# Performance work log

Measured on AMD Instinct MI355X. Metric: run time of the kernel, lower is better.

## Reference

```python
import jax, jax.numpy as jnp
import numpy as np

P = 2; NH = 16; HS = 1024; NL = 12; NC = 1000
B, D, H, W = 32, 64, 32, 32
LFEAT = P * P * D  # 256 per-patch feature dim


def _sincos_1d(dim, pos):
    omega = np.arange(dim // 2, dtype=np.float64) / (dim / 2.0)
    omega = 1.0 / 10000 ** omega
    out = np.einsum('m,d->md', pos.reshape(-1), omega)
    return np.concatenate([np.sin(out), np.cos(out)], axis=1)


def _pos_embed(dim, grid_size):
    g = np.arange(grid_size, dtype=np.float32)
    grid = np.stack(np.meshgrid(g, g), axis=0).reshape(2, 1, grid_size, grid_size)
    emb = np.concatenate([_sincos_1d(dim // 2, grid[0]), _sincos_1d(dim // 2, grid[1])], axis=1)
    return jnp.asarray(emb, dtype=jnp.float32)


def setup_inputs() -> dict:
    key = jax.random.key(0)
    ks = iter(jax.random.split(key, 40))
    def w(shape, s=0.02):
        return jax.random.normal(next(ks), shape, jnp.float32) * s
    return {
        'x': jax.random.normal(next(ks), (B, D, H, W), jnp.float32),
        'y': jax.random.randint(next(ks), (B,), 0, NC),
        't': jax.random.randint(next(ks), (B,), 0, 1000),
        'proj_w': w((LFEAT, HS)), 'proj_b': jnp.zeros((HS,), jnp.float32),
        'pos_embed': _pos_embed(HS, H // P),
        'emb_table': w((NC + 1, HS)),
        'blk_mod_w': w((NL, HS, 6 * HS)), 'blk_mod_b': jnp.zeros((NL, 6 * HS), jnp.float32),
        'blk_wq': w((NL, HS, HS)), 'blk_bq': jnp.zeros((NL, HS), jnp.float32),
        'blk_wk': w((NL, HS, HS)), 'blk_bk': jnp.zeros((NL, HS), jnp.float32),
        'blk_wv': w((NL, HS, HS)), 'blk_bv': jnp.zeros((NL, HS), jnp.float32),
        'blk_wo': w((NL, HS, HS)), 'blk_bo': jnp.zeros((NL, HS), jnp.float32),
        'blk_fc1_w': w((NL, HS, 4 * HS)), 'blk_fc1_b': jnp.zeros((NL, 4 * HS), jnp.float32),
        'blk_fc2_w': w((NL, 4 * HS, HS)), 'blk_fc2_b': jnp.zeros((NL, HS), jnp.float32),
        'fin_mod_w': w((HS, 2 * HS)), 'fin_mod_b': jnp.zeros((2 * HS,), jnp.float32),
        'fin_out_w': w((HS, LFEAT)), 'fin_out_b': jnp.zeros((LFEAT,), jnp.float32),
    }


def _ln(z):
    mu = jnp.mean(z, -1, keepdims=True)
    var = jnp.mean((z - mu) ** 2, -1, keepdims=True)
    return (z - mu) * jax.lax.rsqrt(var + 1e-5)


def _forward(x, y, t, proj_w, proj_b, pos_embed, emb_table,
             blk_mod_w, blk_mod_b, blk_wq, blk_bq, blk_wk, blk_bk, blk_wv, blk_bv,
             blk_wo, blk_bo, blk_fc1_w, blk_fc1_b, blk_fc2_w, blk_fc2_b,
             fin_mod_w, fin_mod_b, fin_out_w, fin_out_b):
    Bc, Dc, Hc, Wc = x.shape
    Hp, Wp = Hc // P, Wc // P
    dh = HS // NH
    # patchify_flatten: (B, L, P*P*D)
    tok = x.reshape(Bc, Dc, Hp, P, Wp, P).transpose(0, 2, 4, 3, 5, 1).reshape(Bc, Hp * Wp, P * P * Dc)
    tok = tok @ proj_w + proj_b + pos_embed[None]
    # timestep_embedding: [cos, sin] order per source
    half = HS // 2
    freqs = jnp.exp(-jnp.log(jnp.float32(10000.0)) * jnp.arange(half, dtype=jnp.float32) / half)
    ang = t.astype(jnp.float32)[:, None] * freqs[None]
    c = jnp.concatenate([jnp.cos(ang), jnp.sin(ang)], axis=-1) + emb_table[y]
    c_act = jax.nn.silu(c)  # each block applies silu to c (c is not mutated across blocks)

    def block(xc, p):
        mw, mb, wq, bq, wk, bk, wv, bv, wo, bo, f1w, f1b, f2w, f2b = p
        mod = c_act @ mw + mb
        sh_a, sc_a, g_a, sh_m, sc_m, g_m = jnp.split(mod, 6, axis=1)
        hx = _ln(xc) * (1 + sc_a[:, None]) + sh_a[:, None]
        def heads(z, wz, bz):
            return (z @ wz + bz).reshape(Bc, -1, NH, dh).transpose(0, 2, 1, 3)
        q, k, v = heads(hx, wq, bq), heads(hx, wk, bk), heads(hx, wv, bv)
        logits = jnp.einsum('bhqd,bhkd->bhqk', q, k) / jnp.sqrt(jnp.float32(dh))
        # non-AR mask buffer is all zeros -> no-op
        attn = jax.nn.softmax(logits, axis=-1)
        o = jnp.einsum('bhqk,bhkd->bhqd', attn, v).transpose(0, 2, 1, 3).reshape(Bc, -1, HS)
        xc = xc + g_a[:, None] * (o @ wo + bo)
        hx = _ln(xc) * (1 + sc_m[:, None]) + sh_m[:, None]
        mlp = jax.nn.gelu(hx @ f1w + f1b, approximate=False) @ f2w + f2b
        return xc + g_m[:, None] * mlp, None

    tok, _ = jax.lax.scan(block, tok, (blk_mod_w, blk_mod_b, blk_wq, blk_bq, blk_wk, blk_bk,
                                       blk_wv, blk_bv, blk_wo, blk_bo,
                                       blk_fc1_w, blk_fc1_b, blk_fc2_w, blk_fc2_b))
    fmod = c_act @ fin_mod_w + fin_mod_b
    sh, sc = jnp.split(fmod, 2, axis=1)
    out = (_ln(tok) * (1 + sc[:, None]) + sh[:, None]) @ fin_out_w + fin_out_b
    # unpatchify -> (B, D, H, W)
    return out.reshape(Bc, Hp, Wp, P, P, Dc).transpose(0, 5, 1, 3, 2, 4).reshape(Bc, Dc, Hc, Wc)


def reference(x, y, t, proj_w, proj_b, pos_embed, emb_table,
              blk_mod_w, blk_mod_b, blk_wq, blk_bq, blk_wk, blk_bk, blk_wv, blk_bv,
              blk_wo, blk_bo, blk_fc1_w, blk_fc1_b, blk_fc2_w, blk_fc2_b,
              fin_mod_w, fin_mod_b, fin_out_w, fin_out_b):
    return _forward(x, y, t, proj_w, proj_b, pos_embed, emb_table,
                    blk_mod_w, blk_mod_b, blk_wq, blk_bq, blk_wk, blk_bk, blk_wv, blk_bv,
                    blk_wo, blk_bo, blk_fc1_w, blk_fc1_b, blk_fc2_w, blk_fc2_b,
                    fin_mod_w, fin_mod_b, fin_out_w, fin_out_b)
```

## Files before the change

kernel.cpp:

```cpp
#include <hip/hip_runtime.h>
#include <hip/hip_bf16.h>
#include <math.h>

typedef short s16x8 __attribute__((ext_vector_type(8)));
typedef float f32x4 __attribute__((ext_vector_type(4)));
typedef unsigned short u16;

__device__ __forceinline__ u16 f2b(float f) {
    unsigned u = __builtin_bit_cast(unsigned, f);
    u += 0x7fffu + ((u >> 16) & 1u);
    return (u16)(u >> 16);
}
__device__ __forceinline__ f32x4 mfma16(s16x8 a, s16x8 b, f32x4 c) {
    return __builtin_amdgcn_mfma_f32_16x16x32_bf16(a, b, c, 0, 0, 0);
}
__device__ __forceinline__ void gload16(const void* g, void* l) {
    __builtin_amdgcn_global_load_lds((const __attribute__((address_space(1))) unsigned*)g,
                                     (__attribute__((address_space(3))) unsigned*)l, 16, 0, 0);
}

__global__ __launch_bounds__(256) void patchify_kernel(const float* __restrict__ x, u16* __restrict__ out) {
    int idx = blockIdx.x * 256 + threadIdx.x;
    int row = idx >> 8, col = idx & 255;
    int b = row >> 8, ll = row & 255, hp = ll >> 4, wp = ll & 15;
    int pp = col >> 6, d = col & 63;
    out[idx] = f2b(x[(size_t)((b * 64 + d) * 32 + hp * 2 + (pp >> 1)) * 32 + wp * 2 + (pp & 1)]);
}

__global__ __launch_bounds__(256) void cact_kernel(const int* __restrict__ t, const int* __restrict__ y,
                                                   const float* __restrict__ emb, u16* __restrict__ cact) {
    int b = blockIdx.x, tid = threadIdx.x;
    float tv = (float)t[b];
    int yb = y[b];
#pragma unroll
    for (int j = 0; j < 4; ++j) {
        int c = tid * 4 + j;
        int f = (c < 512) ? c : c - 512;
        float freq = __expf(-9.210340371976184f * (float)f * (1.f / 512.f));
        float ang = tv * freq;
        float v = (c < 512) ? cosf(ang) : sinf(ang);
        v += emb[(size_t)yb * 1024 + c];
        v = v / (1.f + __expf(-v));
        cact[b * 1024 + c] = f2b(v);
    }
}

__global__ __launch_bounds__(256) void bcat_kernel(const float* __restrict__ bq, const float* __restrict__ bk,
                                                   const float* __restrict__ bv, float* __restrict__ out) {
    int lyr = blockIdx.x, j = blockIdx.y, tid = threadIdx.x;
    const float* src = (j == 0) ? bq : ((j == 1) ? bk : bv);
    float4 v = ((const float4*)(src + (size_t)lyr * 1024))[tid];
    ((float4*)(out + (size_t)lyr * 3072 + j * 1024))[tid] = v;
}

__device__ __forceinline__ void tpose_body(float (*tile)[65], const float* __restrict__ in,
                                           u16* __restrict__ out, int R, int C, int r0, int c0, int tid) {
    int rr = tid >> 4, cc = (tid & 15) * 4;
#pragma unroll
    for (int j = 0; j < 4; ++j) {
        float4 v = *(const float4*)&in[(size_t)(r0 + j * 16 + rr) * C + c0 + cc];
        tile[j * 16 + rr][cc]     = v.x;
        tile[j * 16 + rr][cc + 1] = v.y;
        tile[j * 16 + rr][cc + 2] = v.z;
        tile[j * 16 + rr][cc + 3] = v.w;
    }
    __syncthreads();
    int oc = tid >> 3, r8 = (tid & 7) * 8;
#pragma unroll
    for (int j = 0; j < 2; ++j) {
        int ocl = j * 32 + oc;
        s16x8 vv;
#pragma unroll
        for (int e = 0; e < 8; ++e) vv[e] = (short)f2b(tile[r8 + e][ocl]);
        *(s16x8*)&out[(size_t)(c0 + ocl) * R + r0 + r8] = vv;
    }
}

__global__ __launch_bounds__(256) void transpose_cvt64k(const float* __restrict__ in, u16* __restrict__ out,
                                                        int R, int C) {
    __shared__ float tile[64][65];
    tpose_body(tile, in, out, R, C, blockIdx.y * 64, blockIdx.x * 64, threadIdx.x);
}

__global__ __launch_bounds__(256) void transpose_layer(
    const float* __restrict__ mw, const float* __restrict__ wq, const float* __restrict__ wk,
    const float* __restrict__ wv, const float* __restrict__ wo, const float* __restrict__ f1,
    const float* __restrict__ f2,
    u16* __restrict__ modT, u16* __restrict__ qkvT, u16* __restrict__ woT,
    u16* __restrict__ f1T, u16* __restrict__ f2T) {
    __shared__ float tile[64][65];
    int bid = blockIdx.x, tid = threadIdx.x;
    const float* src; u16* dst; int R, C, tloc;
    if (bid < 1536)      { src = mw; dst = modT;               R = 1024; C = 6144; tloc = bid; }
    else if (bid < 1792) { src = wq; dst = qkvT;               R = 1024; C = 1024; tloc = bid - 1536; }
    else if (bid < 2048) { src = wk; dst = qkvT + 1024 * 1024; R = 1024; C = 1024; tloc = bid - 1792; }
    else if (bid < 2304) { src = wv; dst = qkvT + 2048 * 1024; R = 1024; C = 1024; tloc = bid - 2048; }
    else if (bid < 2560) { src = wo; dst = woT;                R = 1024; C = 1024; tloc = bid - 2304; }
    else if (bid < 3584) { src = f1; dst = f1T;                R = 1024; C = 4096; tloc = bid - 2560; }
    else                 { src = f2; dst = f2T;                R = 4096; C = 1024; tloc = bid - 3584; }
    int tx = C >> 6;
    int ty = tloc / tx, txi = tloc - ty * tx;
    tpose_body(tile, src, dst, R, C, ty * 64, txi * 64, tid);
}

__global__ __launch_bounds__(256) void ln_mod_kernel(const float* __restrict__ x, const float* __restrict__ modv,
                                                     int mod_ld, int sh_off, int sc_off, u16* __restrict__ out) {
    int row = blockIdx.x, tid = threadIdx.x, b = row >> 8;
    float4 xv = ((const float4*)(x + (size_t)row * 1024))[tid];
    float s = xv.x + xv.y + xv.z + xv.w;
    float s2 = xv.x * xv.x + xv.y * xv.y + xv.z * xv.z + xv.w * xv.w;
#pragma unroll
    for (int d = 1; d < 64; d <<= 1) { s += __shfl_xor(s, d); s2 += __shfl_xor(s2, d); }
    __shared__ float red[8];
    int w = tid >> 6;
    if ((tid & 63) == 0) { red[w] = s; red[4 + w] = s2; }
    __syncthreads();
    s = red[0] + red[1] + red[2] + red[3];
    s2 = red[4] + red[5] + red[6] + red[7];
    float mu = s * (1.f / 1024.f);
    float rs = rsqrtf(s2 * (1.f / 1024.f) - mu * mu + 1e-5f);
    const float* shp = modv + (size_t)b * mod_ld + sh_off;
    const float* scp = modv + (size_t)b * mod_ld + sc_off;
    float4 sh4 = ((const float4*)shp)[tid];
    float4 sc4 = ((const float4*)scp)[tid];
    u16 o0 = f2b((xv.x - mu) * rs * (1.f + sc4.x) + sh4.x);
    u16 o1 = f2b((xv.y - mu) * rs * (1.f + sc4.y) + sh4.y);
    u16 o2 = f2b((xv.z - mu) * rs * (1.f + sc4.z) + sh4.z);
    u16 o3 = f2b((xv.w - mu) * rs * (1.f + sc4.w) + sh4.w);
    unsigned long long pk = (unsigned long long)o0 | ((unsigned long long)o1 << 16) |
                            ((unsigned long long)o2 << 32) | ((unsigned long long)o3 << 48);
    *(unsigned long long*)&out[(size_t)row * 1024 + tid * 4] = pk;
}

template <int EPI>
__global__ __launch_bounds__(512, 1) void gemm8(
    const u16* __restrict__ A, int lda, const u16* __restrict__ Bt, int ldb,
    int M, int N, int K, const float* __restrict__ bias,
    float* __restrict__ outF, u16* __restrict__ outB, int ldc,
    const float* __restrict__ aux1, const float* __restrict__ aux2, int gateOff) {
    __shared__ u16 As[3][256 * 64];
    __shared__ u16 Bs[3][128 * 64];

    const int tid = threadIdx.x, w = tid >> 6, l = tid & 63;
    const int wm = w >> 1, wn = w & 1;

    const int nbn = N >> 7;
    const int nwg = gridDim.x;
    const int orig = blockIdx.x;
    const int cpx = nwg >> 3;
    const int wg = (orig & 7) * cpx + (orig >> 3);
    const int bm = wg / nbn, bn = wg - bm * nbn;
    const int row0 = bm << 8, col0 = bn << 7;

    const int NT = K >> 6;

    const int srow = tid >> 3, sslot = tid & 7;
    const int ksl = sslot ^ (((srow >> 2) & 1) << 1);
    const u16* gA = A + (size_t)(row0 + srow) * lda + ksl * 8;
    const u16* gB = Bt + (size_t)(col0 + srow) * ldb + ksl * 8;
    const int lOff = srow * 64 + sslot * 8;

    const int fr = l & 15, fg = l >> 4;
    const int arow = wm * 64 + fr;
    const int brow = wn * 64 + fr;

    f32x4 acc[4][4];
#pragma unroll
    for (int m = 0; m < 4; ++m)
#pragma unroll
        for (int n = 0; n < 4; ++n) acc[m][n] = (f32x4){0.f, 0.f, 0.f, 0.f};

    {
        u16* a0 = &As[0][lOff];
        u16* b0 = &Bs[0][lOff];
#pragma unroll
        for (int a = 0; a < 4; ++a) gload16(gA + (size_t)a * 64 * lda, a0 + a * 4096);
#pragma unroll
        for (int b = 0; b < 2; ++b) gload16(gB + (size_t)b * 64 * ldb, b0 + b * 4096);
        if (NT > 1) {
            u16* a1 = &As[1][lOff];
#pragma unroll
            for (int a = 0; a < 3; ++a) gload16(gA + (size_t)a * 64 * lda + 64, a1 + a * 4096);
        }
    }
    if (NT > 1) { asm volatile("s_waitcnt vmcnt(3)" ::: "memory"); }
    else        { asm volatile("s_waitcnt vmcnt(0)" ::: "memory"); }
    __builtin_amdgcn_s_barrier();
    __builtin_amdgcn_sched_barrier(0);

    int q = 0;
    for (int t = 0; t < NT; ++t) {
        const u16* ca = As[q];
        const u16* cb = Bs[q];
        const int q1 = (q == 2) ? 0 : q + 1;
        const int q2 = (q1 == 2) ? 0 : q1 + 1;

        s16x8 af[4][2], bf[4][2];
#pragma unroll
        for (int m = 0; m < 4; ++m) {
            int r = arow + m * 16;
            int psb = fg ^ (((r >> 2) & 1) << 1);
            af[m][0] = *(const s16x8*)(ca + r * 64 + psb * 8);
            af[m][1] = *(const s16x8*)(ca + r * 64 + psb * 8 + 32);
        }
#pragma unroll
        for (int n = 0; n < 2; ++n) {
            int r = brow + n * 16;
            int psb = fg ^ (((r >> 2) & 1) << 1);
            bf[n][0] = *(const s16x8*)(cb + r * 64 + psb * 8);
            bf[n][1] = *(const s16x8*)(cb + r * 64 + psb * 8 + 32);
        }
        if (t + 1 < NT) {
            gload16(gA + (size_t)(3 * 64) * lda + (size_t)(t + 1) * 64, &As[q1][lOff] + 3 * 4096);
            gload16(gB + (size_t)(t + 1) * 64, &Bs[q1][lOff]);
            gload16(gB + (size_t)(1 * 64) * ldb + (size_t)(t + 1) * 64, &Bs[q1][lOff] + 4096);
        }
        __builtin_amdgcn_s_barrier();
        __builtin_amdgcn_s_setprio(1);
#pragma unroll
        for (int m = 0; m < 4; ++m)
#pragma unroll
            for (int n = 0; n < 2; ++n) {
                acc[m][n] = mfma16(af[m][0], bf[n][0], acc[m][n]);
                acc[m][n] = mfma16(af[m][1], bf[n][1], acc[m][n]);
            }
        __builtin_amdgcn_s_setprio(0);
        __builtin_amdgcn_s_barrier();
#pragma unroll
        for (int n = 0; n < 2; ++n) {
            int r = brow + (n + 2) * 16;
            int psb = fg ^ (((r >> 2) & 1) << 1);
            bf[n + 2][0] = *(const s16x8*)(cb + r * 64 + psb * 8);
            bf[n + 2][1] = *(const s16x8*)(cb + r * 64 + psb * 8 + 32);
        }
        if (t + 2 < NT) {
#pragma unroll
            for (int a = 0; a < 3; ++a)
                gload16(gA + (size_t)a * 64 * lda + (size_t)(t + 2) * 64, &As[q2][lOff] + a * 4096);
        }
        __builtin_amdgcn_s_barrier();
        __builtin_amdgcn_s_setprio(1);
#pragma unroll
        for (int m = 0; m < 4; ++m)
#pragma unroll
            for (int n = 2; n < 4; ++n) {
                acc[m][n] = mfma16(af[m][0], bf[n][0], acc[m][n]);
                acc[m][n] = mfma16(af[m][1], bf[n][1], acc[m][n]);
            }
        __builtin_amdgcn_s_setprio(0);
        if (t < NT - 2)       { asm volatile("s_waitcnt vmcnt(3)" ::: "memory"); }
        else if (t == NT - 2) { asm volatile("s_waitcnt vmcnt(0)" ::: "memory"); }
        if (t < NT - 1) {
            __builtin_amdgcn_s_barrier();
            __builtin_amdgcn_sched_barrier(0);
        }
        q = q1;
    }

    const int erow = row0 + wm * 64 + fg * 4;
    const int ecol = col0 + wn * 64 + fr;
#pragma unroll
    for (int m = 0; m < 4; ++m) {
#pragma unroll
        for (int n = 0; n < 4; ++n) {
#pragma unroll
            for (int r = 0; r < 4; ++r) {
                int row = erow + m * 16 + r;
                int col = ecol + n * 16;
                float v = acc[m][n][r];
                if constexpr (EPI == 1) {
                    outB[(size_t)row * ldc + col] = f2b(v + bias[col]);
                } else if constexpr (EPI == 2) {
                    outF[(size_t)row * ldc + col] = v + bias[col] + aux1[(size_t)(row & 255) * 1024 + col];
                } else if constexpr (EPI == 3) {
                    outF[(size_t)row * ldc + col] =
                        aux1[(size_t)row * ldc + col] +
                        aux2[(size_t)(row >> 8) * 6144 + gateOff + col] * (v + bias[col]);
                } else {
                    float xg = v + bias[col];
                    outB[(size_t)row * ldc + col] = f2b(0.5f * xg * (1.f + erff(xg * 0.70710678118654752f)));
                }
            }
        }
    }
}

template <int EPI>
__global__ __launch_bounds__(256, 2) void gemm_k(
    const u16* __restrict__ A, int lda, const u16* __restrict__ Bt, int ldb,
    int M, int N, int K, const float* __restrict__ bias,
    float* outF, u16* __restrict__ outB, int ldc) {
    __shared__ u16 Asl[128 * 32];
    __shared__ u16 Bsl[128 * 32];
    const int tid = threadIdx.x, w = tid >> 6, l = tid & 63;
    const int row0 = blockIdx.y * 128, col0 = blockIdx.x * 128;
    const int wm = w >> 1, wn = w & 1;

    f32x4 acc[4][4];
#pragma unroll
    for (int m = 0; m < 4; ++m)
#pragma unroll
        for (int n = 0; n < 4; ++n) acc[m][n] = (f32x4){0.f, 0.f, 0.f, 0.f};

    const int rA0 = w * 16 + (l >> 2), rA1 = rA0 + 64;
    const int kc = (l & 3) * 8;
    int gr0 = row0 + rA0; if (gr0 > M - 1) gr0 = M - 1;
    int gr1 = row0 + rA1; if (gr1 > M - 1) gr1 = M - 1;
    const u16* a0 = A + (size_t)gr0 * lda + kc;
    const u16* a1 = A + (size_t)gr1 * lda + kc;
    const u16* b0 = Bt + (size_t)(col0 + rA0) * ldb + kc;
    const u16* b1 = Bt + (size_t)(col0 + rA1) * ldb + kc;
    u16* la0 = &Asl[rA0 * 32 + kc];
    u16* la1 = &Asl[rA1 * 32 + kc];
    u16* lb0 = &Bsl[rA0 * 32 + kc];
    u16* lb1 = &Bsl[rA1 * 32 + kc];

    for (int k0 = 0; k0 < K; k0 += 32) {
        __syncthreads();
        gload16(a0 + k0, la0);
        gload16(a1 + k0, la1);
        gload16(b0 + k0, lb0);
        gload16(b1 + k0, lb1);
        __syncthreads();
        s16x8 af[4], bfr[4];
#pragma unroll
        for (int m = 0; m < 4; ++m)
            af[m] = *(const s16x8*)&Asl[(wm * 64 + m * 16 + (l & 15)) * 32 + (l >> 4) * 8];
#pragma unroll
        for (int n = 0; n < 4; ++n)
            bfr[n] = *(const s16x8*)&Bsl[(wn * 64 + n * 16 + (l & 15)) * 32 + (l >> 4) * 8];
#pragma unroll
        for (int m = 0; m < 4; ++m)
#pragma unroll
            for (int n = 0; n < 4; ++n) acc[m][n] = mfma16(af[m], bfr[n], acc[m][n]);
    }

#pragma unroll
    for (int m = 0; m < 4; ++m) {
#pragma unroll
        for (int n = 0; n < 4; ++n) {
#pragma unroll
            for (int r = 0; r < 4; ++r) {
                int row = row0 + wm * 64 + m * 16 + (l >> 4) * 4 + r;
                if (row >= M) continue;
                int col = col0 + wn * 64 + n * 16 + (l & 15);
                float v = acc[m][n][r];
                if constexpr (EPI == 0) {
                    outF[(size_t)row * ldc + col] = v + bias[col];
                } else {
                    float xg = v + bias[col];
                    int bb = row >> 8, ll = row & 255, hp = ll >> 4, wp = ll & 15;
                    int pp = col >> 6, d = col & 63;
                    outF[(size_t)((bb * 64 + d) * 32 + hp * 2 + (pp >> 1)) * 32 + wp * 2 + (pp & 1)] = xg;
                }
            }
        }
    }
}

__global__ __launch_bounds__(256, 2) void attn_kernel(const u16* __restrict__ qkv, u16* __restrict__ obuf) {
    __shared__ u16 Qs[64 * 64];
    __shared__ u16 Ks[256 * 64];
    __shared__ u16 VTs[64 * 256];
    int qt = blockIdx.x, h = blockIdx.y, b = blockIdx.z;
    int tid = threadIdx.x, w = tid >> 6, l = tid & 63;
    size_t base = (size_t)b * 256 * 3072;

    {
        int r = tid >> 2;
#pragma unroll
        for (int j = 0; j < 2; ++j) {
            int sg = (tid & 3) + j * 4;
            *(s16x8*)&Qs[r * 64 + sg * 8] =
                *(const s16x8*)&qkv[base + (size_t)(qt * 64 + r) * 3072 + h * 64 + sg * 8];
        }
    }
#pragma unroll
    for (int j = 0; j < 8; ++j) {
        int i = tid + j * 256;
        int r = i >> 3, sg = i & 7;
        *(s16x8*)&Ks[r * 64 + sg * 8] =
            *(const s16x8*)&qkv[base + (size_t)r * 3072 + 1024 + h * 64 + sg * 8];
    }
#pragma unroll
    for (int j = 0; j < 8; ++j) {
        int i = tid + j * 256;
        int r = i >> 3, sg = i & 7;
        s16x8 v = *(const s16x8*)&qkv[base + (size_t)r * 3072 + 2048 + h * 64 + sg * 8];
#pragma unroll
        for (int e = 0; e < 8; ++e) VTs[(sg * 8 + e) * 256 + r] = ((const u16*)&v)[e];
    }
    __syncthreads();

    s16x8 aq0 = *(const s16x8*)&Qs[(w * 16 + (l & 15)) * 64 + (l >> 4) * 8];
    s16x8 aq1 = *(const s16x8*)&Qs[(w * 16 + (l & 15)) * 64 + 32 + (l >> 4) * 8];
    f32x4 sf[16];
#pragma unroll
    for (int cf = 0; cf < 16; ++cf) {
        f32x4 a = (f32x4){0.f, 0.f, 0.f, 0.f};
        s16x8 bk0 = *(const s16x8*)&Ks[(cf * 16 + (l & 15)) * 64 + (l >> 4) * 8];
        s16x8 bk1 = *(const s16x8*)&Ks[(cf * 16 + (l & 15)) * 64 + 32 + (l >> 4) * 8];
        a = mfma16(aq0, bk0, a);
        a = mfma16(aq1, bk1, a);
        sf[cf] = a * 0.125f;
    }
    __syncthreads();

#pragma unroll
    for (int r = 0; r < 4; ++r) {
        float m = -1e30f;
#pragma unroll
        for (int cf = 0; cf < 16; ++cf) m = fmaxf(m, sf[cf][r]);
#pragma unroll
        for (int d = 1; d < 16; d <<= 1) m = fmaxf(m, __shfl_xor(m, d));
        float sm = 0.f;
#pragma unroll
        for (int cf = 0; cf < 16; ++cf) { float e = __expf(sf[cf][r] - m); sf[cf][r] = e; sm += e; }
#pragma unroll
        for (int d = 1; d < 16; d <<= 1) sm += __shfl_xor(sm, d);
        float inv = 1.f / sm;
        int rl = w * 16 + (l >> 4) * 4 + r;
#pragma unroll
        for (int cf = 0; cf < 16; ++cf) Ks[rl * 256 + cf * 16 + (l & 15)] = f2b(sf[cf][r] * inv);
    }
    __syncthreads();

    f32x4 oacc[4];
#pragma unroll
    for (int cf = 0; cf < 4; ++cf) oacc[cf] = (f32x4){0.f, 0.f, 0.f, 0.f};
#pragma unroll
    for (int ks = 0; ks < 8; ++ks) {
        s16x8 ap = *(const s16x8*)&Ks[(w * 16 + (l & 15)) * 256 + ks * 32 + (l >> 4) * 8];
#pragma unroll
        for (int cf = 0; cf < 4; ++cf) {
            s16x8 bv = *(const s16x8*)&VTs[(cf * 16 + (l & 15)) * 256 + ks * 32 + (l >> 4) * 8];
            oacc[cf] = mfma16(ap, bv, oacc[cf]);
        }
    }
    size_t orow0 = (size_t)(b * 256 + qt * 64 + w * 16);
#pragma unroll
    for (int cf = 0; cf < 4; ++cf)
#pragma unroll
        for (int r = 0; r < 4; ++r) {
            int rr = (l >> 4) * 4 + r;
            obuf[(orow0 + rr) * 1024 + h * 64 + cf * 16 + (l & 15)] = f2b(oacc[cf][r]);
        }
}

extern "C" void kernel_launch(void* const* d_in, const int* in_sizes, int n_in,
                              void* d_out, int out_size, void* d_ws, size_t ws_size,
                              hipStream_t stream) {
    (void)in_sizes; (void)n_in; (void)out_size; (void)ws_size;
    const float* x         = (const float*)d_in[0];
    const int*   y         = (const int*)d_in[1];
    const int*   t         = (const int*)d_in[2];
    const float* proj_w    = (const float*)d_in[3];
    const float* proj_b    = (const float*)d_in[4];
    const float* pos_embed = (const float*)d_in[5];
    const float* emb_table = (const float*)d_in[6];
    const float* blk_mod_w = (const float*)d_in[7];
    const float* blk_mod_b = (const float*)d_in[8];
    const float* blk_wq    = (const float*)d_in[9];
    const float* blk_bq    = (const float*)d_in[10];
    const float* blk_wk    = (const float*)d_in[11];
    const float* blk_bk    = (const float*)d_in[12];
    const float* blk_wv    = (const float*)d_in[13];
    const float* blk_bv    = (const float*)d_in[14];
    const float* blk_wo    = (const float*)d_in[15];
    const float* blk_bo    = (const float*)d_in[16];
    const float* blk_f1w   = (const float*)d_in[17];
    const float* blk_f1b   = (const float*)d_in[18];
    const float* blk_f2w   = (const float*)d_in[19];
    const float* blk_f2b   = (const float*)d_in[20];
    const float* fin_mod_w = (const float*)d_in[21];
    const float* fin_mod_b = (const float*)d_in[22];
    const float* fin_out_w = (const float*)d_in[23];
    const float* fin_out_b = (const float*)d_in[24];
    float* out = (float*)d_out;

    char* ws = (char*)d_ws;
    size_t off = 0;
    auto alloc = [&](size_t bytes) -> char* {
        char* p = ws + off;
        off += (bytes + 255) & ~(size_t)255;
        return p;
    };
    float* xc    = (float*)alloc(8192ull * 1024 * 4);
    u16*   hx    = (u16*)alloc(8192ull * 1024 * 2);
    u16*   qkvb  = (u16*)alloc(8192ull * 3072 * 2);
    u16*   obufp = (u16*)alloc(8192ull * 1024 * 2);
    u16*   h1    = (u16*)alloc(8192ull * 4096 * 2);
    u16*   patchA= (u16*)alloc(8192ull * 256 * 2);
    u16*   cact  = (u16*)alloc(32ull * 1024 * 2);
    float* modb  = (float*)alloc(32ull * 6144 * 4);
    float* fmod  = (float*)alloc(32ull * 2048 * 4);
    float* bqkv  = (float*)alloc(12ull * 3072 * 4);
    u16*   projT = (u16*)alloc(1024ull * 256 * 2);
    u16*   fmT   = (u16*)alloc(2048ull * 1024 * 2);
    u16*   foT   = (u16*)alloc(256ull * 1024 * 2);
    u16*   modT  = (u16*)alloc(6144ull * 1024 * 2);
    u16*   qkvT  = (u16*)alloc(3072ull * 1024 * 2);
    u16*   woT   = (u16*)alloc(1024ull * 1024 * 2);
    u16*   f1T   = (u16*)alloc(4096ull * 1024 * 2);
    u16*   f2T   = (u16*)alloc(1024ull * 4096 * 2);

    patchify_kernel<<<8192, 256, 0, stream>>>(x, patchA);
    cact_kernel<<<32, 256, 0, stream>>>(t, y, emb_table, cact);
    bcat_kernel<<<dim3(12, 3), 256, 0, stream>>>(blk_bq, blk_bk, blk_bv, bqkv);
    transpose_cvt64k<<<dim3(16, 4), 256, 0, stream>>>(proj_w, projT, 256, 1024);
    transpose_cvt64k<<<dim3(32, 16), 256, 0, stream>>>(fin_mod_w, fmT, 1024, 2048);
    transpose_cvt64k<<<dim3(4, 16), 256, 0, stream>>>(fin_out_w, foT, 1024, 256);

    gemm8<2><<<256, 512, 0, stream>>>(patchA, 256, projT, 256, 8192, 1024, 256,
                                      proj_b, xc, nullptr, 1024, pos_embed, nullptr, 0);
    gemm_k<0><<<dim3(16, 1), 256, 0, stream>>>(cact, 1024, fmT, 1024, 32, 2048, 1024,
                                               fin_mod_b, fmod, nullptr, 2048);

    for (int i = 0; i < 12; ++i) {
        transpose_layer<<<4608, 256, 0, stream>>>(
            blk_mod_w + (size_t)i * 1024 * 6144,
            blk_wq + (size_t)i * 1024 * 1024, blk_wk + (size_t)i * 1024 * 1024,
            blk_wv + (size_t)i * 1024 * 1024, blk_wo + (size_t)i * 1024 * 1024,
            blk_f1w + (size_t)i * 1024 * 4096, blk_f2w + (size_t)i * 4096 * 1024,
            modT, qkvT, woT, f1T, f2T);

        gemm_k<0><<<dim3(48, 1), 256, 0, stream>>>(cact, 1024, modT, 1024, 32, 6144, 1024,
                                                   blk_mod_b + (size_t)i * 6144, modb, nullptr, 6144);
        ln_mod_kernel<<<8192, 256, 0, stream>>>(xc, modb, 6144, 0, 1024, hx);
        gemm8<1><<<768, 512, 0, stream>>>(hx, 1024, qkvT, 1024, 8192, 3072, 1024,
                                          bqkv + (size_t)i * 3072, nullptr, qkvb, 3072,
                                          nullptr, nullptr, 0);
        attn_kernel<<<dim3(4, 16, 32), 256, 0, stream>>>(qkvb, obufp);
        gemm8<3><<<256, 512, 0, stream>>>(obufp, 1024, woT, 1024, 8192, 1024, 1024,
                                          blk_bo + (size_t)i * 1024, xc, nullptr, 1024,
                                          xc, modb, 2048);
        ln_mod_kernel<<<8192, 256, 0, stream>>>(xc, modb, 6144, 3072, 4096, hx);
        gemm8<4><<<1024, 512, 0, stream>>>(hx, 1024, f1T, 1024, 8192, 4096, 1024,
                                           blk_f1b + (size_t)i * 4096, nullptr, h1, 4096,
                                           nullptr, nullptr, 0);
        gemm8<3><<<256, 512, 0, stream>>>(h1, 4096, f2T, 4096, 8192, 1024, 4096,
                                          blk_f2b + (size_t)i * 1024, xc, nullptr, 1024,
                                          xc, modb, 5120);
    }
    ln_mod_kernel<<<8192, 256, 0, stream>>>(xc, fmod, 2048, 0, 1024, hx);
    gemm_k<5><<<dim3(2, 64), 256, 0, stream>>>(hx, 1024, foT, 1024, 8192, 256, 1024,
                                               fin_out_b, out, nullptr, 256);
}
```

Measured before the change: 5.103 ms.

## Add 256x256 GEMM for QKV/FC1, fp32 mod GEMV, drop mod-weight transpose

Adds a gemm256 kernel with 256x256 tiles and K-step 32 for the QKV and FC1 projections, so each workgroup reuses more data per LDS load than the 256x128 gemm8. The adaLN modulation matmuls (M=32) move to a new fp32 mod32_kernel that reads the untransposed weights directly. This removes the per-layer transpose and bf16 conversion of the large 1024x6144 mod weight. gemm8's LDS swizzle changes to a full 8-slot XOR to cut bank conflicts. The fp32 GEMV is bandwidth bound and still reads the full fp32 weight; the larger tiles cut the number of workgroups.

```diff
diff --git a/kernel.cpp b/kernel.cpp
--- a/kernel.cpp
+++ b/kernel.cpp
@@ -28,7 +28,7 @@
 }
 
 __global__ __launch_bounds__(256) void cact_kernel(const int* __restrict__ t, const int* __restrict__ y,
-                                                   const float* __restrict__ emb, u16* __restrict__ cact) {
+                                                   const float* __restrict__ emb, float* __restrict__ cactF) {
     int b = blockIdx.x, tid = threadIdx.x;
     float tv = (float)t[b];
     int yb = y[b];
@@ -41,7 +41,7 @@
         float v = (c < 512) ? cosf(ang) : sinf(ang);
         v += emb[(size_t)yb * 1024 + c];
         v = v / (1.f + __expf(-v));
-        cact[b * 1024 + c] = f2b(v);
+        cactF[b * 1024 + c] = v;
     }
 }
 
@@ -53,6 +53,51 @@
     ((float4*)(out + (size_t)lyr * 3072 + j * 1024))[tid] = v;
 }
 
+__global__ __launch_bounds__(256) void mod32_kernel(const float* __restrict__ cactF, const float* __restrict__ W,
+                                                    const float* __restrict__ bias, float* __restrict__ out, int N) {
+    __shared__ float cs[32 * 256];
+    __shared__ float red[4 * 32 * 64];
+    int tid = threadIdx.x, lane = tid & 63, kg = tid >> 6;
+    int n = blockIdx.x * 64 + lane;
+    float acc[32];
+#pragma unroll
+    for (int r = 0; r < 32; ++r) acc[r] = 0.f;
+    for (int ch = 0; ch < 4; ++ch) {
+        __syncthreads();
+#pragma unroll
+        for (int j = 0; j < 8; ++j) {
+            int idx = tid * 4 + j * 1024;
+            float4 v = *(const float4*)&cactF[(size_t)(idx >> 8) * 1024 + ch * 256 + (idx & 255)];
+            *(float4*)&cs[idx] = v;
+        }
+        __syncthreads();
+        const float* Wp = W + (size_t)(ch * 256 + kg * 64) * N + n;
+        for (int kk = 0; kk < 64; kk += 4) {
+            float w0 = Wp[(size_t)(kk + 0) * N];
+            float w1 = Wp[(size_t)(kk + 1) * N];
+            float w2 = Wp[(size_t)(kk + 2) * N];
+            float w3 = Wp[(size_t)(kk + 3) * N];
+            int kb = kg * 64 + kk;
+#pragma unroll
+            for (int r = 0; r < 32; ++r) {
+                float4 cv = *(const float4*)&cs[r * 256 + kb];
+                acc[r] += cv.x * w0 + cv.y * w1 + cv.z * w2 + cv.w * w3;
+            }
+        }
+    }
+#pragma unroll
+    for (int r = 0; r < 32; ++r) red[(kg * 32 + r) * 64 + lane] = acc[r];
+    __syncthreads();
+    int r = tid >> 3, j0 = (tid & 7) * 8;
+#pragma unroll
+    for (int jj = 0; jj < 8; ++jj) {
+        int nn = j0 + jj;
+        float s = red[(0 * 32 + r) * 64 + nn] + red[(1 * 32 + r) * 64 + nn] +
+                  red[(2 * 32 + r) * 64 + nn] + red[(3 * 32 + r) * 64 + nn];
+        out[(size_t)r * N + blockIdx.x * 64 + nn] = s + bias[blockIdx.x * 64 + nn];
+    }
+}
+
 __device__ __forceinline__ void tpose_body(float (*tile)[65], const float* __restrict__ in,
                                            u16* __restrict__ out, int R, int C, int r0, int c0, int tid) {
     int rr = tid >> 4, cc = (tid & 15) * 4;
@@ -83,21 +128,19 @@
 }
 
 __global__ __launch_bounds__(256) void transpose_layer(
-    const float* __restrict__ mw, const float* __restrict__ wq, const float* __restrict__ wk,
+    const float* __restrict__ wq, const float* __restrict__ wk,
     const float* __restrict__ wv, const float* __restrict__ wo, const float* __restrict__ f1,
     const float* __restrict__ f2,
-    u16* __restrict__ modT, u16* __restrict__ qkvT, u16* __restrict__ woT,
-    u16* __restrict__ f1T, u16* __restrict__ f2T) {
+    u16* __restrict__ qkvT, u16* __restrict__ woT, u16* __restrict__ f1T, u16* __restrict__ f2T) {
     __shared__ float tile[64][65];
     int bid = blockIdx.x, tid = threadIdx.x;
     const float* src; u16* dst; int R, C, tloc;
-    if (bid < 1536)      { src = mw; dst = modT;               R = 1024; C = 6144; tloc = bid; }
-    else if (bid < 1792) { src = wq; dst = qkvT;               R = 1024; C = 1024; tloc = bid - 1536; }
-    else if (bid < 2048) { src = wk; dst = qkvT + 1024 * 1024; R = 1024; C = 1024; tloc = bid - 1792; }
-    else if (bid < 2304) { src = wv; dst = qkvT + 2048 * 1024; R = 1024; C = 1024; tloc = bid - 2048; }
-    else if (bid < 2560) { src = wo; dst = woT;                R = 1024; C = 1024; tloc = bid - 2304; }
-    else if (bid < 3584) { src = f1; dst = f1T;                R = 1024; C = 4096; tloc = bid - 2560; }
-    else                 { src = f2; dst = f2T;                R = 4096; C = 1024; tloc = bid - 3584; }
+    if (bid < 256)       { src = wq; dst = qkvT;               R = 1024; C = 1024; tloc = bid; }
+    else if (bid < 512)  { src = wk; dst = qkvT + 1024 * 1024; R = 1024; C = 1024; tloc = bid - 256; }
+    else if (bid < 768)  { src = wv; dst = qkvT + 2048 * 1024; R = 1024; C = 1024; tloc = bid - 512; }
+    else if (bid < 1024) { src = wo; dst = woT;                R = 1024; C = 1024; tloc = bid - 768; }
+    else if (bid < 2048) { src = f1; dst = f1T;                R = 1024; C = 4096; tloc = bid - 1024; }
+    else                 { src = f2; dst = f2T;                R = 4096; C = 1024; tloc = bid - 2048; }
     int tx = C >> 6;
     int ty = tloc / tx, txi = tloc - ty * tx;
     tpose_body(tile, src, dst, R, C, ty * 64, txi * 64, tid);
@@ -133,6 +176,130 @@
 }
 
 template <int EPI>
+__global__ __launch_bounds__(512, 1) void gemm256(
+    const u16* __restrict__ A, int lda, const u16* __restrict__ Bt, int ldb,
+    int M, int N, int K, const float* __restrict__ bias, u16* __restrict__ outB, int ldc) {
+    __shared__ u16 As[3][256 * 32];
+    __shared__ u16 Bs[3][256 * 32];
+
+    const int tid = threadIdx.x, w = tid >> 6, l = tid & 63;
+    const int wm = w >> 1, wn = w & 1;
+    const int fr = l & 15, fg = l >> 4;
+
+    const int nbn = N >> 8;
+    const int orig = blockIdx.x;
+    const int cpx = gridDim.x >> 3;
+    const int wg = (orig & 7) * cpx + (orig >> 3);
+    const int bm = wg / nbn, bn = wg - bm * nbn;
+    const int row0 = bm << 8, col0 = bn << 8;
+    const int NT = K >> 5;
+
+    const int srow = tid >> 2, slot = tid & 3;
+    const int gs = slot ^ ((srow >> 1) & 3);
+    const u16* gA = A + (size_t)(row0 + srow) * lda + gs * 8;
+    const u16* gB = Bt + (size_t)(col0 + srow) * ldb + gs * 8;
+
+    int aoff[4], boff[8];
+#pragma unroll
+    for (int m = 0; m < 4; ++m) {
+        int rr = wm * 64 + m * 16 + fr;
+        aoff[m] = rr * 32 + ((fg ^ ((rr >> 1) & 3)) * 8);
+    }
+#pragma unroll
+    for (int j = 0; j < 8; ++j) {
+        int rr = wn * 128 + j * 16 + fr;
+        boff[j] = rr * 32 + ((fg ^ ((rr >> 1) & 3)) * 8);
+    }
+
+    f32x4 acc[4][8];
+#pragma unroll
+    for (int m = 0; m < 4; ++m)
+#pragma unroll
+        for (int j = 0; j < 8; ++j) acc[m][j] = (f32x4){0.f, 0.f, 0.f, 0.f};
+
+    {
+        u16* d0 = &As[0][tid * 8];
+        gload16(gA, d0); gload16(gA + (size_t)128 * lda, d0 + 4096);
+        u16* e0 = &Bs[0][tid * 8];
+        gload16(gB, e0); gload16(gB + (size_t)128 * ldb, e0 + 4096);
+        u16* d1 = &As[1][tid * 8];
+        gload16(gA + 32, d1); gload16(gA + (size_t)128 * lda + 32, d1 + 4096);
+        u16* e1 = &Bs[1][tid * 8];
+        gload16(gB + 32, e1); gload16(gB + (size_t)128 * ldb + 32, e1 + 4096);
+    }
+    asm volatile("s_waitcnt vmcnt(4)" ::: "memory");
+    __builtin_amdgcn_s_barrier();
+    __builtin_amdgcn_sched_barrier(0);
+
+    int q = 0;
+    for (int t = 0; t < NT; ++t) {
+        const u16* ca = As[q];
+        const u16* cb = Bs[q];
+        const int q1 = (q == 2) ? 0 : q + 1;
+        const int q2 = (q1 == 2) ? 0 : q1 + 1;
+
+        s16x8 af[4], bfv[4];
+#pragma unroll
+        for (int m = 0; m < 4; ++m) af[m] = *(const s16x8*)(ca + aoff[m]);
+#pragma unroll
+        for (int j = 0; j < 4; ++j) bfv[j] = *(const s16x8*)(cb + boff[j]);
+        if (t + 2 < NT) {
+            u16* d = &As[q2][tid * 8];
+            const u16* s = gA + (size_t)(t + 2) * 32;
+            gload16(s, d); gload16(s + (size_t)128 * lda, d + 4096);
+        }
+        __builtin_amdgcn_s_barrier();
+        __builtin_amdgcn_s_setprio(1);
+#pragma unroll
+        for (int m = 0; m < 4; ++m)
+#pragma unroll
+            for (int j = 0; j < 4; ++j) acc[m][j] = mfma16(af[m], bfv[j], acc[m][j]);
+        __builtin_amdgcn_s_setprio(0);
+        __builtin_amdgcn_s_barrier();
+#pragma unroll
+        for (int j = 0; j < 4; ++j) bfv[j] = *(const s16x8*)(cb + boff[j + 4]);
+        if (t + 2 < NT) {
+            u16* d = &Bs[q2][tid * 8];
+            const u16* s = gB + (size_t)(t + 2) * 32;
+            gload16(s, d); gload16(s + (size_t)128 * ldb, d + 4096);
+        }
+        __builtin_amdgcn_s_setprio(1);
+#pragma unroll
+        for (int m = 0; m < 4; ++m)
+#pragma unroll
+            for (int j = 0; j < 4; ++j) acc[m][j + 4] = mfma16(af[m], bfv[j], acc[m][j + 4]);
+        __builtin_amdgcn_s_setprio(0);
+        if (t < NT - 2)       { asm volatile("s_waitcnt vmcnt(4)" ::: "memory"); }
+        else if (t == NT - 2) { asm volatile("s_waitcnt vmcnt(0)" ::: "memory"); }
+        if (t < NT - 1) {
+            __builtin_amdgcn_s_barrier();
+            __builtin_amdgcn_sched_barrier(0);
+        }
+        q = q1;
+    }
+
+    const int erow = row0 + wm * 64 + fg * 4;
+    const int ecol = col0 + wn * 128 + fr;
+#pragma unroll
+    for (int m = 0; m < 4; ++m) {
+#pragma unroll
+        for (int j = 0; j < 8; ++j) {
+#pragma unroll
+            for (int r = 0; r < 4; ++r) {
+                int row = erow + m * 16 + r;
+                int col = ecol + j * 16;
+                float v = acc[m][j][r] + bias[col];
+                if constexpr (EPI == 1) {
+                    outB[(size_t)row * ldc + col] = f2b(v);
+                } else {
+                    outB[(size_t)row * ldc + col] = f2b(0.5f * v * (1.f + erff(v * 0.70710678118654752f)));
+                }
+            }
+        }
+    }
+}
+
+template <int EPI>
 __global__ __launch_bounds__(512, 1) void gemm8(
     const u16* __restrict__ A, int lda, const u16* __restrict__ Bt, int ldb,
     int M, int N, int K, const float* __restrict__ bias,
@@ -145,9 +312,8 @@
     const int wm = w >> 1, wn = w & 1;
 
     const int nbn = N >> 7;
-    const int nwg = gridDim.x;
     const int orig = blockIdx.x;
-    const int cpx = nwg >> 3;
+    const int cpx = gridDim.x >> 3;
     const int wg = (orig & 7) * cpx + (orig >> 3);
     const int bm = wg / nbn, bn = wg - bm * nbn;
     const int row0 = bm << 8, col0 = bn << 7;
@@ -155,7 +321,7 @@
     const int NT = K >> 6;
 
     const int srow = tid >> 3, sslot = tid & 7;
-    const int ksl = sslot ^ (((srow >> 2) & 1) << 1);
+    const int ksl = sslot ^ (srow & 7);
     const u16* gA = A + (size_t)(row0 + srow) * lda + ksl * 8;
     const u16* gB = Bt + (size_t)(col0 + srow) * ldb + ksl * 8;
     const int lOff = srow * 64 + sslot * 8;
@@ -199,16 +365,14 @@
 #pragma unroll
         for (int m = 0; m < 4; ++m) {
             int r = arow + m * 16;
-            int psb = fg ^ (((r >> 2) & 1) << 1);
-            af[m][0] = *(const s16x8*)(ca + r * 64 + psb * 8);
-            af[m][1] = *(const s16x8*)(ca + r * 64 + psb * 8 + 32);
+            af[m][0] = *(const s16x8*)(ca + r * 64 + ((fg     ^ (r & 7)) * 8));
+            af[m][1] = *(const s16x8*)(ca + r * 64 + (((4 + fg) ^ (r & 7)) * 8));
         }
 #pragma unroll
         for (int n = 0; n < 2; ++n) {
             int r = brow + n * 16;
-            int psb = fg ^ (((r >> 2) & 1) << 1);
-            bf[n][0] = *(const s16x8*)(cb + r * 64 + psb * 8);
-            bf[n][1] = *(const s16x8*)(cb + r * 64 + psb * 8 + 32);
+            bf[n][0] = *(const s16x8*)(cb + r * 64 + ((fg     ^ (r & 7)) * 8));
+            bf[n][1] = *(const s16x8*)(cb + r * 64 + (((4 + fg) ^ (r & 7)) * 8));
         }
         if (t + 1 < NT) {
             gload16(gA + (size_t)(3 * 64) * lda + (size_t)(t + 1) * 64, &As[q1][lOff] + 3 * 4096);
@@ -229,9 +393,8 @@
 #pragma unroll
         for (int n = 0; n < 2; ++n) {
             int r = brow + (n + 2) * 16;
-            int psb = fg ^ (((r >> 2) & 1) << 1);
-            bf[n + 2][0] = *(const s16x8*)(cb + r * 64 + psb * 8);
-            bf[n + 2][1] = *(const s16x8*)(cb + r * 64 + psb * 8 + 32);
+            bf[n + 2][0] = *(const s16x8*)(cb + r * 64 + ((fg     ^ (r & 7)) * 8));
+            bf[n + 2][1] = *(const s16x8*)(cb + r * 64 + (((4 + fg) ^ (r & 7)) * 8));
         }
         if (t + 2 < NT) {
 #pragma unroll
@@ -268,28 +431,21 @@
                 int row = erow + m * 16 + r;
                 int col = ecol + n * 16;
                 float v = acc[m][n][r];
-                if constexpr (EPI == 1) {
-                    outB[(size_t)row * ldc + col] = f2b(v + bias[col]);
-                } else if constexpr (EPI == 2) {
+                if constexpr (EPI == 2) {
                     outF[(size_t)row * ldc + col] = v + bias[col] + aux1[(size_t)(row & 255) * 1024 + col];
-                } else if constexpr (EPI == 3) {
+                } else {
                     outF[(size_t)row * ldc + col] =
                         aux1[(size_t)row * ldc + col] +
                         aux2[(size_t)(row >> 8) * 6144 + gateOff + col] * (v + bias[col]);
-                } else {
-                    float xg = v + bias[col];
-                    outB[(size_t)row * ldc + col] = f2b(0.5f * xg * (1.f + erff(xg * 0.70710678118654752f)));
                 }
             }
         }
     }
 }
 
-template <int EPI>
-__global__ __launch_bounds__(256, 2) void gemm_k(
+__global__ __launch_bounds__(256, 2) void gemm_fin(
     const u16* __restrict__ A, int lda, const u16* __restrict__ Bt, int ldb,
-    int M, int N, int K, const float* __restrict__ bias,
-    float* outF, u16* __restrict__ outB, int ldc) {
+    int M, int N, int K, const float* __restrict__ bias, float* outF) {
     __shared__ u16 Asl[128 * 32];
     __shared__ u16 Bsl[128 * 32];
     const int tid = threadIdx.x, w = tid >> 6, l = tid & 63;
@@ -304,10 +460,8 @@
 
     const int rA0 = w * 16 + (l >> 2), rA1 = rA0 + 64;
     const int kc = (l & 3) * 8;
-    int gr0 = row0 + rA0; if (gr0 > M - 1) gr0 = M - 1;
-    int gr1 = row0 + rA1; if (gr1 > M - 1) gr1 = M - 1;
-    const u16* a0 = A + (size_t)gr0 * lda + kc;
-    const u16* a1 = A + (size_t)gr1 * lda + kc;
+    const u16* a0 = A + (size_t)(row0 + rA0) * lda + kc;
+    const u16* a1 = A + (size_t)(row0 + rA1) * lda + kc;
     const u16* b0 = Bt + (size_t)(col0 + rA0) * ldb + kc;
     const u16* b1 = Bt + (size_t)(col0 + rA1) * ldb + kc;
     u16* la0 = &Asl[rA0 * 32 + kc];
@@ -342,17 +496,11 @@
 #pragma unroll
             for (int r = 0; r < 4; ++r) {
                 int row = row0 + wm * 64 + m * 16 + (l >> 4) * 4 + r;
-                if (row >= M) continue;
                 int col = col0 + wn * 64 + n * 16 + (l & 15);
-                float v = acc[m][n][r];
-                if constexpr (EPI == 0) {
-                    outF[(size_t)row * ldc + col] = v + bias[col];
-                } else {
-                    float xg = v + bias[col];
-                    int bb = row >> 8, ll = row & 255, hp = ll >> 4, wp = ll & 15;
-                    int pp = col >> 6, d = col & 63;
-                    outF[(size_t)((bb * 64 + d) * 32 + hp * 2 + (pp >> 1)) * 32 + wp * 2 + (pp & 1)] = xg;
-                }
+                float xg = acc[m][n][r] + bias[col];
+                int bb = row >> 8, ll = row & 255, hp = ll >> 4, wp = ll & 15;
+                int pp = col >> 6, d = col & 63;
+                outF[(size_t)((bb * 64 + d) * 32 + hp * 2 + (pp >> 1)) * 32 + wp * 2 + (pp & 1)] = xg;
             }
         }
     }
@@ -491,58 +639,51 @@
     u16*   obufp = (u16*)alloc(8192ull * 1024 * 2);
     u16*   h1    = (u16*)alloc(8192ull * 4096 * 2);
     u16*   patchA= (u16*)alloc(8192ull * 256 * 2);
-    u16*   cact  = (u16*)alloc(32ull * 1024 * 2);
+    float* cactF = (float*)alloc(32ull * 1024 * 4);
     float* modb  = (float*)alloc(32ull * 6144 * 4);
     float* fmod  = (float*)alloc(32ull * 2048 * 4);
     float* bqkv  = (float*)alloc(12ull * 3072 * 4);
     u16*   projT = (u16*)alloc(1024ull * 256 * 2);
-    u16*   fmT   = (u16*)alloc(2048ull * 1024 * 2);
     u16*   foT   = (u16*)alloc(256ull * 1024 * 2);
-    u16*   modT  = (u16*)alloc(6144ull * 1024 * 2);
     u16*   qkvT  = (u16*)alloc(3072ull * 1024 * 2);
     u16*   woT   = (u16*)alloc(1024ull * 1024 * 2);
     u16*   f1T   = (u16*)alloc(4096ull * 1024 * 2);
     u16*   f2T   = (u16*)alloc(1024ull * 4096 * 2);
 
     patchify_kernel<<<8192, 256, 0, stream>>>(x, patchA);
-    cact_kernel<<<32, 256, 0, stream>>>(t, y, emb_table, cact);
+    cact_kernel<<<32, 256, 0, stream>>>(t, y, emb_table, cactF);
     bcat_kernel<<<dim3(12, 3), 256, 0, stream>>>(blk_bq, blk_bk, blk_bv, bqkv);
     transpose_cvt64k<<<dim3(16, 4), 256, 0, stream>>>(proj_w, projT, 256, 1024);
-    transpose_cvt64k<<<dim3(32, 16), 256, 0, stream>>>(fin_mod_w, fmT, 1024, 2048);
     transpose_cvt64k<<<dim3(4, 16), 256, 0, stream>>>(fin_out_w, foT, 1024, 256);
+    mod32_kernel<<<32, 256, 0, stream>>>(cactF, fin_mod_w, fin_mod_b, fmod, 2048);
 
     gemm8<2><<<256, 512, 0, stream>>>(patchA, 256, projT, 256, 8192, 1024, 256,
                                       proj_b, xc, nullptr, 1024, pos_embed, nullptr, 0);
-    gemm_k<0><<<dim3(16, 1), 256, 0, stream>>>(cact, 1024, fmT, 1024, 32, 2048, 1024,
-                                               fin_mod_b, fmod, nullptr, 2048);
 
     for (int i = 0; i < 12; ++i) {
-        transpose_layer<<<4608, 256, 0, stream>>>(
-            blk_mod_w + (size_t)i * 1024 * 6144,
+        transpose_layer<<<3072, 256, 0, stream>>>(
             blk_wq + (size_t)i * 1024 * 1024, blk_wk + (size_t)i * 1024 * 1024,
             blk_wv + (size_t)i * 1024 * 1024, blk_wo + (size_t)i * 1024 * 1024,
             blk_f1w + (size_t)i * 1024 * 4096, blk_f2w + (size_t)i * 4096 * 1024,
-            modT, qkvT, woT, f1T, f2T);
-
-        gemm_k<0><<<dim3(48, 1), 256, 0, stream>>>(cact, 1024, modT, 1024, 32, 6144, 1024,
-                                                   blk_mod_b + (size_t)i * 6144, modb, nullptr, 6144);
+            qkvT, woT, f1T, f2T);
+
+        mod32_kernel<<<96, 256, 0, stream>>>(cactF, blk_mod_w + (size_t)i * 1024 * 6144,
+                                             blk_mod_b + (size_t)i * 6144, modb, 6144);
         ln_mod_kernel<<<8192, 256, 0, stream>>>(xc, modb, 6144, 0, 1024, hx);
-        gemm8<1><<<768, 512, 0, stream>>>(hx, 1024, qkvT, 1024, 8192, 3072, 1024,
-                                          bqkv + (size_t)i * 3072, nullptr, qkvb, 3072,
-                                          nullptr, nullptr, 0);
+        gemm256<1><<<384, 512, 0, stream>>>(hx, 1024, qkvT, 1024, 8192, 3072, 1024,
+                                            bqkv + (size_t)i * 3072, qkvb, 3072);
         attn_kernel<<<dim3(4, 16, 32), 256, 0, stream>>>(qkvb, obufp);
         gemm8<3><<<256, 512, 0, stream>>>(obufp, 1024, woT, 1024, 8192, 1024, 1024,
                                           blk_bo + (size_t)i * 1024, xc, nullptr, 1024,
                                           xc, modb, 2048);
         ln_mod_kernel<<<8192, 256, 0, stream>>>(xc, modb, 6144, 3072, 4096, hx);
-        gemm8<4><<<1024, 512, 0, stream>>>(hx, 1024, f1T, 1024, 8192, 4096, 1024,
-                                           blk_f1b + (size_t)i * 4096, nullptr, h1, 4096,
-                                           nullptr, nullptr, 0);
+        gemm256<4><<<512, 512, 0, stream>>>(hx, 1024, f1T, 1024, 8192, 4096, 1024,
+                                            blk_f1b + (size_t)i * 4096, h1, 4096);
         gemm8<3><<<256, 512, 0, stream>>>(h1, 4096, f2T, 4096, 8192, 1024, 4096,
                                           blk_f2b + (size_t)i * 1024, xc, nullptr, 1024,
                                           xc, modb, 5120);
     }
     ln_mod_kernel<<<8192, 256, 0, stream>>>(xc, fmod, 2048, 0, 1024, hx);
-    gemm_k<5><<<dim3(2, 64), 256, 0, stream>>>(hx, 1024, foT, 1024, 8192, 256, 1024,
-                                               fin_out_b, out, nullptr, 256);
-}
+    gemm_fin<<<dim3(2, 64), 256, 0, stream>>>(hx, 1024, foT, 1024, 8192, 256, 1024,
+                                              fin_out_b, out);
+}
```

After: 6.159 ms. +20.7%, slower.
